# Performance work log

Hardware: AMD Instinct MI355X
Metric: run time of the kernel (lower is better)

Reference implementation:

```python
import jax, jax.numpy as jnp
import numpy as np

B, N, D, K = 4, 4096, 128, 20

def setup_inputs() -> dict:
    key = jax.random.key(0)
    k1, k2, k3 = jax.random.split(key, 3)
    s = 1.0 / np.sqrt(D)
    return {
        "x": jax.random.normal(k1, (B, N, D), dtype=jnp.float32),
        "Wq": jax.random.normal(k2, (D, D), dtype=jnp.float32) * s,
        "bq": jnp.zeros((D,), dtype=jnp.float32),
        "Wk": jax.random.normal(k3, (D, D), dtype=jnp.float32) * s,
        "bk": jnp.zeros((D,), dtype=jnp.float32),
    }

def reference(x, Wq, bq, Wk, bk):
    # Q/K projections: [B,N,D]
    Q = jnp.einsum('bnd,de->bne', x, Wq) + bq
    Kp = jnp.einsum('bnd,de->bne', x, Wk) + bk
    # scores: [B,N,N], scaled by sqrt(D)
    attn = jnp.einsum('bnd,bmd->bnm', Q, Kp) / jnp.sqrt(jnp.float32(D))
    # top-k along last dim -> binary mask via scatter
    _, topk_idx = jax.lax.top_k(attn, K)  # [B,N,K]
    bi = jnp.arange(B)[:, None, None]
    ni = jnp.arange(N)[None, :, None]
    mask = jnp.zeros_like(attn).at[bi, ni, topk_idx].set(1.0)
    # zero out non-topk entries, then full softmax over all N (zeros included,
    # matching the torch module exactly)
    sparse_attn = attn * mask
    out = jax.nn.softmax(sparse_attn, axis=-1)
    return out[..., None]  # [B,N,N,1]
```

## Files before the change

### kernel.cpp

```cpp
#include <hip/hip_runtime.h>

#define BN 4096
#define BD 128
#define NB 4
#define TOPK 20
#define CAND 96
#define EPS_U 0.9f

typedef float f32x16 __attribute__((ext_vector_type(16)));
typedef short bf16x8 __attribute__((ext_vector_type(8)));

__device__ inline unsigned short f2bf(float f) {
  unsigned int u = __float_as_uint(f);
  unsigned int r = (u + 0x7FFFu + ((u >> 16) & 1u)) >> 16;
  return (unsigned short)r;
}

__global__ __launch_bounds__(256) void proj_kernel(
    const float* __restrict__ x,
    const float* __restrict__ Wq, const float* __restrict__ bq,
    const float* __restrict__ Wk, const float* __restrict__ bk,
    double* __restrict__ Qd, double* __restrict__ Kd, unsigned short* __restrict__ Khi) {
  __shared__ double xs[32][129];
  const int tid = threadIdx.x;
  const long row0 = (long)blockIdx.x * 32;
  const float* xsrc = x + row0 * BD;
  for (int i = tid; i < 32 * BD; i += 256) xs[i >> 7][i & 127] = (double)xsrc[i];
  __syncthreads();

  const int e = tid & 127;
  const bool isK = tid >= 128;
  const float* W = isK ? Wk : Wq;
  const float* bias = isK ? bk : bq;
  double* Od = isK ? Kd : Qd;

  double acc[32];
  const double binit = (double)bias[e];
#pragma unroll
  for (int r = 0; r < 32; ++r) acc[r] = binit;

  for (int d = 0; d < BD; ++d) {
    const double wv = (double)W[d * BD + e];
#pragma unroll
    for (int r = 0; r < 32; ++r) acc[r] = fma(xs[r][d], wv, acc[r]);
  }

#pragma unroll
  for (int r = 0; r < 32; ++r) {
    const double a = acc[r];
    const long o = (row0 + r) * BD + e;
    Od[o] = a;
    if (isK) Khi[o] = f2bf((float)a);
  }
}

__global__ __launch_bounds__(512) void screen_kernel(
    const double* __restrict__ Qd, const unsigned short* __restrict__ Khi,
    unsigned short* __restrict__ Sbf) {
  __shared__ char sbuf[8][2560];

  const int tid = threadIdx.x;
  const int lane = tid & 63;
  const int w = tid >> 6;
  const int kt = w & 3, qt = w >> 2;
  const int c31 = lane & 31, hi = lane >> 5;

  const int blk = blockIdx.x;
  const int xcd = blk & 7;
  const int j = blk >> 3;
  const int combo = xcd * 2 + (j & 1);
  const int b = combo >> 2;
  const int kq = combo & 3;
  const int rg = j >> 1;
  const int rowbase = rg << 6;
  const int kvbase = kq << 10;

  const int qrow = qt * 32 + c31;
  const long grow = (long)b * BN + rowbase + qrow;

  bf16x8 bqf[8];
  {
    const double* qp = Qd + grow * BD + hi * 8;
#pragma unroll
    for (int ks = 0; ks < 8; ++ks) {
      bf16x8 pk;
#pragma unroll
      for (int jj = 0; jj < 8; ++jj) pk[jj] = (short)f2bf((float)qp[ks * 16 + jj]);
      bqf[ks] = pk;
    }
  }

  const unsigned short* kb = Khi + ((long)b * BN + kvbase + kt * 32 + c31) * BD + hi * 8;
  char* my = sbuf[w];
  const int wr = c31 * 80;

  const long gq = (long)b * BN + rowbase + qt * 32 + (lane >> 1);
  unsigned short* dstbase = Sbf + gq * BN + kvbase + kt * 32 + (lane & 1) * 16;
  const char* rdp = my + (lane >> 1) * 80 + (lane & 1) * 32;

  for (int step = 0; step < 8; ++step) {
    const unsigned short* kr = kb + (long)step * 128 * BD;
    f32x16 acc = {0.f, 0.f, 0.f, 0.f, 0.f, 0.f, 0.f, 0.f,
                  0.f, 0.f, 0.f, 0.f, 0.f, 0.f, 0.f, 0.f};
#pragma unroll
    for (int ks = 0; ks < 8; ++ks) {
      const bf16x8 a = *(const bf16x8*)(kr + ks * 16);
      acc = __builtin_amdgcn_mfma_f32_32x32x16_bf16(a, bqf[ks], acc, 0, 0, 0);
    }

#pragma unroll
    for (int p = 0; p < 4; ++p) {
      const unsigned int lo =
          (unsigned int)f2bf(acc[p * 4 + 0]) | ((unsigned int)f2bf(acc[p * 4 + 1]) << 16);
      const unsigned int hi2 =
          (unsigned int)f2bf(acc[p * 4 + 2]) | ((unsigned int)f2bf(acc[p * 4 + 3]) << 16);
      *(uint2*)(my + wr + p * 16 + hi * 8) = make_uint2(lo, hi2);
    }
    const uint4 r0 = *(const uint4*)(rdp);
    const uint4 r1 = *(const uint4*)(rdp + 16);
    unsigned short* dst = dstbase + step * 128;
    *(uint4*)dst = r0;
    *(uint4*)(dst + 8) = r1;
  }
}

__device__ inline float rescore_f64(const double2* __restrict__ kp2, const double2* __restrict__ q2) {
  double a0 = 0.0, a1 = 0.0, a2 = 0.0, a3 = 0.0;
#pragma unroll
  for (int i = 0; i < 64; i += 4) {
    a0 = fma(q2[i + 0].y, kp2[i + 0].y, fma(q2[i + 0].x, kp2[i + 0].x, a0));
    a1 = fma(q2[i + 1].y, kp2[i + 1].y, fma(q2[i + 1].x, kp2[i + 1].x, a1));
    a2 = fma(q2[i + 2].y, kp2[i + 2].y, fma(q2[i + 2].x, kp2[i + 2].x, a2));
    a3 = fma(q2[i + 3].y, kp2[i + 3].y, fma(q2[i + 3].x, kp2[i + 3].x, a3));
  }
  return (float)(((a0 + a1) + (a2 + a3)) * 8.8388347648318447e-02);
}

__device__ inline unsigned int fmono(float v) {
  const unsigned int u = __float_as_uint(v);
  return (u & 0x80000000u) ? ~u : (u | 0x80000000u);
}
__device__ inline float fdemono(unsigned int k) {
  const unsigned int u = (k & 0x80000000u) ? (k & 0x7fffffffu) : ~k;
  return __uint_as_float(u);
}

__global__ __launch_bounds__(256) void topk_kernel(
    const double* __restrict__ Qd, const double* __restrict__ Kd,
    const unsigned short* __restrict__ Sbf, unsigned int* __restrict__ rec) {
  __shared__ unsigned short listL[4][CAND];
  __shared__ unsigned int cntL[4];

  const int tid = threadIdx.x;
  const int lane = tid & 63;
  const int w = tid >> 6;
  const int blk = blockIdx.x;
  const int b = (blk & 7) >> 1;
  const int idx = ((blk >> 3) << 1) | (blk & 1);
  const long row = (long)b * BN + idx * 4 + w;

  const unsigned short* srow = Sbf + row * BN;

  uint4 v[8];
  float pm[8];
#pragma unroll
  for (int i = 0; i < 8; ++i) {
    v[i] = *(const uint4*)(srow + i * 512 + lane * 8);
    float m0 = -3.4e38f;
#pragma unroll
    for (int k = 0; k < 4; ++k) {
      const unsigned int u = (&v[i].x)[k];
      m0 = fmaxf(m0, fmaxf(__uint_as_float(u << 16), __uint_as_float(u & 0xFFFF0000u)));
    }
    pm[i] = m0;
  }
  float mymax = fmaxf(fmaxf(fmaxf(pm[0], pm[1]), fmaxf(pm[2], pm[3])),
                      fmaxf(fmaxf(pm[4], pm[5]), fmaxf(pm[6], pm[7])));

  float vb = mymax;
#pragma unroll
  for (int k = 2; k <= 64; k <<= 1) {
#pragma unroll
    for (int jj = k >> 1; jj > 0; jj >>= 1) {
      const float o = __shfl_xor(vb, jj);
      const bool keepmin = (((lane & k) == 0) == ((lane & jj) == 0));
      vb = keepmin ? fminf(vb, o) : fmaxf(vb, o);
    }
  }
  const float th = __shfl(vb, 44) - EPS_U;

  if (lane == 0) cntL[w] = 0;

#pragma unroll
  for (int i = 0; i < 8; ++i) {
#pragma unroll
    for (int k = 0; k < 4; ++k) {
      const unsigned int u = (&v[i].x)[k];
      const float f0 = __uint_as_float(u << 16);
      const float f1 = __uint_as_float(u & 0xFFFF0000u);
      const int col0 = i * 512 + lane * 8 + k * 2;
      if (f0 >= th) {
        const unsigned int p = atomicAdd(&cntL[w], 1u);
        if (p < CAND) listL[w][p] = (unsigned short)col0;
      }
      if (f1 >= th) {
        const unsigned int p = atomicAdd(&cntL[w], 1u);
        if (p < CAND) listL[w][p] = (unsigned short)(col0 + 1);
      }
    }
  }

  const int c = (int)min(cntL[w], (unsigned int)CAND);

  const double2* q2 = (const double2*)(Qd + row * BD);
  const double* kbd = Kd + (long)b * BN * BD;

  unsigned long long key0 = 0ull, key1 = 0ull;
  if (lane < c) {
    const int kv = (int)listL[w][lane];
    const float vv = rescore_f64((const double2*)(kbd + (long)kv * BD), q2);
    key0 = ((unsigned long long)fmono(vv) << 12) | (unsigned int)(4095 - kv);
  }
  if (lane + 64 < c) {
    const int kv = (int)listL[w][lane + 64];
    const float vv = rescore_f64((const double2*)(kbd + (long)kv * BD), q2);
    key1 = ((unsigned long long)fmono(vv) << 12) | (unsigned int)(4095 - kv);
  }

  unsigned int* rr = rec + row * 48;

  if (c <= 64) {
    unsigned long long kk = key0;
#pragma unroll
    for (int k = 2; k <= 64; k <<= 1) {
#pragma unroll
      for (int jj = k >> 1; jj > 0; jj >>= 1) {
        const unsigned long long o = __shfl_xor(kk, jj);
        const bool keepmin = (((lane & k) == 0) == ((lane & jj) == 0));
        kk = keepmin ? (o < kk ? o : kk) : (o > kk ? o : kk);
      }
    }
    const unsigned long long ktop = __shfl(kk, 63);
    const float m = fmaxf(fdemono((unsigned int)(ktop >> 12)), 0.0f);
    const float val = fdemono((unsigned int)(kk >> 12));
    const int col = 4095 - (int)(kk & 0xFFFull);
    const float e = (lane >= 44) ? expf(val - m) : 0.0f;
    float se = e;
#pragma unroll
    for (int off = 32; off; off >>= 1) se += __shfl_xor(se, off);
    const float Z = se + (float)(BN - TOPK) * expf(-m);
    if (lane >= 44) {
      const int r = 63 - lane;
      rr[r] = __float_as_uint(e / Z);
      rr[20 + r] = (unsigned int)col;
    }
    if (lane == 0) rr[40] = __float_as_uint(expf(-m) / Z);
  } else {
    if (key1 > key0) { const unsigned long long t = key0; key0 = key1; key1 = t; }
    float m = 0.0f, se = 0.0f;
    float myval = 0.0f;
    int mycol = 0;
    for (int it = 0; it < TOPK; ++it) {
      unsigned long long rk = key0;
      for (int off = 32; off; off >>= 1) {
        const unsigned long long ok = __shfl_xor(rk, off);
        rk = (ok > rk) ? ok : rk;
      }
      const float rv = fdemono((unsigned int)(rk >> 12));
      if (it == 0) m = fmaxf(rv, 0.0f);
      se += expf(rv - m);
      if (lane == it) { myval = rv; mycol = 4095 - (int)(rk & 0xFFFull); }
      if (key0 == rk) { key0 = key1; key1 = 0ull; }
    }
    const float Z = se + (float)(BN - TOPK) * expf(-m);
    if (lane < TOPK) {
      rr[lane] = __float_as_uint(expf(myval - m) / Z);
      rr[20 + lane] = (unsigned int)mycol;
    }
    if (lane == 0) rr[40] = __float_as_uint(expf(-m) / Z);
  }
}

__global__ __launch_bounds__(256) void fill_kernel(
    const unsigned int* __restrict__ rec, float* __restrict__ out) {
  __shared__ unsigned int bm[128];
  __shared__ float pv[TOPK];
  __shared__ int pc[TOPK];
  __shared__ float sc0;

  const int tid = threadIdx.x;
  const long row = blockIdx.x;
  const unsigned int* rr = rec + row * 48;

  if (tid < 128) bm[tid] = 0;
  __syncthreads();
  if (tid < TOPK) {
    pv[tid] = __uint_as_float(rr[tid]);
    const int col = (int)rr[20 + tid];
    pc[tid] = col;
    atomicOr(&bm[col >> 5], 1u << (col & 31));
  }
  if (tid == TOPK) sc0 = __uint_as_float(rr[40]);
  __syncthreads();

  const float c0 = sc0;
  const float4 cv = make_float4(c0, c0, c0, c0);
  float4* op = (float4*)(out + row * BN);

#pragma unroll
  for (int k = 0; k < 4; ++k) {
    const int j = tid + k * 256;
    const unsigned int bits = (bm[j >> 3] >> ((j & 7) * 4)) & 0xFu;
    if (bits == 0u) {
      op[j] = cv;
    } else {
      float4 v = cv;
      const int col0 = j * 4;
#pragma unroll
      for (int cmp = 0; cmp < 4; ++cmp) {
        if ((bits >> cmp) & 1u) {
          const int col = col0 + cmp;
          float pvv = c0;
          for (int i = 0; i < TOPK; ++i)
            if (pc[i] == col) pvv = pv[i];
          (&v.x)[cmp] = pvv;
        }
      }
      op[j] = v;
    }
  }
}

extern "C" void kernel_launch(void* const* d_in, const int* in_sizes, int n_in,
                              void* d_out, int out_size, void* d_ws, size_t ws_size,
                              hipStream_t stream) {
  const float* x  = (const float*)d_in[0];
  const float* Wq = (const float*)d_in[1];
  const float* bq = (const float*)d_in[2];
  const float* Wk = (const float*)d_in[3];
  const float* bk = (const float*)d_in[4];
  float* out = (float*)d_out;

  const long NE = (long)NB * BN * BD;
  const long NR = (long)NB * BN;
  double* Qd = (double*)d_ws;
  double* Kd = Qd + NE;
  unsigned short* Khi = (unsigned short*)(Kd + NE);
  unsigned short* Sbf = Khi + NE;
  unsigned int* rec = (unsigned int*)(Sbf + NR * BN);

  proj_kernel<<<NB * BN / 32, 256, 0, stream>>>(x, Wq, bq, Wk, bk, Qd, Kd, Khi);
  screen_kernel<<<1024, 512, 0, stream>>>(Qd, Khi, Sbf);
  topk_kernel<<<NR / 4, 256, 0, stream>>>(Qd, Kd, Sbf, rec);
  fill_kernel<<<NR, 256, 0, stream>>>(rec, out);
}
```

Before: 326.0 us.

## Fuse screening GEMM and top-k selection into one kernel with in-register threshold

Merges the bf16 MFMA screening kernel and the top-k rescoring kernel into a single kernel where each block owns 32 query rows across all 4096 keys. While computing scores, each lane keeps a running top-2, and these are pooled in shared memory and bitonic-sorted to derive the candidate threshold, replacing the separate full-row max pass. Candidate compaction now uses wave ballots and popcount instead of LDS atomics. The block still writes and then rereads the bf16 score rows. The grid shrinks to 512 blocks, so parallelism per block and launch occupancy change.

```diff
diff --git a/kernel.cpp b/kernel.cpp
--- a/kernel.cpp
+++ b/kernel.cpp
@@ -54,33 +54,49 @@
   }
 }
 
-__global__ __launch_bounds__(512) void screen_kernel(
-    const double* __restrict__ Qd, const unsigned short* __restrict__ Khi,
-    unsigned short* __restrict__ Sbf) {
+__device__ inline float rescore_f64(const double2* __restrict__ kp2, const double2* __restrict__ q2) {
+  double a0 = 0.0, a1 = 0.0, a2 = 0.0, a3 = 0.0;
+#pragma unroll
+  for (int i = 0; i < 64; i += 4) {
+    a0 = fma(q2[i + 0].y, kp2[i + 0].y, fma(q2[i + 0].x, kp2[i + 0].x, a0));
+    a1 = fma(q2[i + 1].y, kp2[i + 1].y, fma(q2[i + 1].x, kp2[i + 1].x, a1));
+    a2 = fma(q2[i + 2].y, kp2[i + 2].y, fma(q2[i + 2].x, kp2[i + 2].x, a2));
+    a3 = fma(q2[i + 3].y, kp2[i + 3].y, fma(q2[i + 3].x, kp2[i + 3].x, a3));
+  }
+  return (float)(((a0 + a1) + (a2 + a3)) * 8.8388347648318447e-02);
+}
+
+__device__ inline unsigned int fmono(float v) {
+  const unsigned int u = __float_as_uint(v);
+  return (u & 0x80000000u) ? ~u : (u | 0x80000000u);
+}
+__device__ inline float fdemono(unsigned int k) {
+  const unsigned int u = (k & 0x80000000u) ? (k & 0x7fffffffu) : ~k;
+  return __uint_as_float(u);
+}
+
+__global__ __launch_bounds__(512) void fused_kernel(
+    const double* __restrict__ Qd, const double* __restrict__ Kd,
+    const unsigned short* __restrict__ Khi,
+    unsigned short* __restrict__ Sbf, unsigned int* __restrict__ rec) {
   __shared__ char sbuf[8][2560];
+  __shared__ float pool[32][32];
+  __shared__ float tauL[32];
+  __shared__ unsigned short listL[8][CAND];
 
   const int tid = threadIdx.x;
   const int lane = tid & 63;
   const int w = tid >> 6;
-  const int kt = w & 3, qt = w >> 2;
   const int c31 = lane & 31, hi = lane >> 5;
 
   const int blk = blockIdx.x;
-  const int xcd = blk & 7;
-  const int j = blk >> 3;
-  const int combo = xcd * 2 + (j & 1);
-  const int b = combo >> 2;
-  const int kq = combo & 3;
-  const int rg = j >> 1;
-  const int rowbase = rg << 6;
-  const int kvbase = kq << 10;
-
-  const int qrow = qt * 32 + c31;
-  const long grow = (long)b * BN + rowbase + qrow;
+  const int b = (blk & 7) >> 1;
+  const int rg = ((blk >> 3) << 1) | (blk & 1);
+  const int rowbase = rg << 5;
 
   bf16x8 bqf[8];
   {
-    const double* qp = Qd + grow * BD + hi * 8;
+    const double* qp = Qd + ((long)b * BN + rowbase + c31) * BD + hi * 8;
 #pragma unroll
     for (int ks = 0; ks < 8; ++ks) {
       bf16x8 pk;
@@ -90,16 +106,18 @@
     }
   }
 
-  const unsigned short* kb = Khi + ((long)b * BN + kvbase + kt * 32 + c31) * BD + hi * 8;
+  const unsigned short* kb = Khi + ((long)b * BN + w * 512 + c31) * BD + hi * 8;
+
   char* my = sbuf[w];
   const int wr = c31 * 80;
-
-  const long gq = (long)b * BN + rowbase + qt * 32 + (lane >> 1);
-  unsigned short* dstbase = Sbf + gq * BN + kvbase + kt * 32 + (lane & 1) * 16;
+  unsigned short* dstbase = Sbf + ((long)b * BN + rowbase + (lane >> 1)) * BN
+                            + w * 512 + (lane & 1) * 16;
   const char* rdp = my + (lane >> 1) * 80 + (lane & 1) * 32;
 
-  for (int step = 0; step < 8; ++step) {
-    const unsigned short* kr = kb + (long)step * 128 * BD;
+  float t1 = -3.4e38f, t2 = -3.4e38f;
+
+  for (int t = 0; t < 16; ++t) {
+    const unsigned short* kr = kb + (long)t * 32 * BD;
     f32x16 acc = {0.f, 0.f, 0.f, 0.f, 0.f, 0.f, 0.f, 0.f,
                   0.f, 0.f, 0.f, 0.f, 0.f, 0.f, 0.f, 0.f};
 #pragma unroll
@@ -107,7 +125,13 @@
       const bf16x8 a = *(const bf16x8*)(kr + ks * 16);
       acc = __builtin_amdgcn_mfma_f32_32x32x16_bf16(a, bqf[ks], acc, 0, 0, 0);
     }
-
+#pragma unroll
+    for (int reg = 0; reg < 16; ++reg) {
+      const float s = acc[reg];
+      const float w1 = fmaxf(t1, s);
+      t2 = fmaxf(t2, fminf(t1, s));
+      t1 = w1;
+    }
 #pragma unroll
     for (int p = 0; p < 4; ++p) {
       const unsigned int lo =
@@ -118,166 +142,135 @@
     }
     const uint4 r0 = *(const uint4*)(rdp);
     const uint4 r1 = *(const uint4*)(rdp + 16);
-    unsigned short* dst = dstbase + step * 128;
+    unsigned short* dst = dstbase + t * 32;
     *(uint4*)dst = r0;
     *(uint4*)(dst + 8) = r1;
   }
-}
-
-__device__ inline float rescore_f64(const double2* __restrict__ kp2, const double2* __restrict__ q2) {
-  double a0 = 0.0, a1 = 0.0, a2 = 0.0, a3 = 0.0;
-#pragma unroll
-  for (int i = 0; i < 64; i += 4) {
-    a0 = fma(q2[i + 0].y, kp2[i + 0].y, fma(q2[i + 0].x, kp2[i + 0].x, a0));
-    a1 = fma(q2[i + 1].y, kp2[i + 1].y, fma(q2[i + 1].x, kp2[i + 1].x, a1));
-    a2 = fma(q2[i + 2].y, kp2[i + 2].y, fma(q2[i + 2].x, kp2[i + 2].x, a2));
-    a3 = fma(q2[i + 3].y, kp2[i + 3].y, fma(q2[i + 3].x, kp2[i + 3].x, a3));
-  }
-  return (float)(((a0 + a1) + (a2 + a3)) * 8.8388347648318447e-02);
-}
-
-__device__ inline unsigned int fmono(float v) {
-  const unsigned int u = __float_as_uint(v);
-  return (u & 0x80000000u) ? ~u : (u | 0x80000000u);
-}
-__device__ inline float fdemono(unsigned int k) {
-  const unsigned int u = (k & 0x80000000u) ? (k & 0x7fffffffu) : ~k;
-  return __uint_as_float(u);
-}
-
-__global__ __launch_bounds__(256) void topk_kernel(
-    const double* __restrict__ Qd, const double* __restrict__ Kd,
-    const unsigned short* __restrict__ Sbf, unsigned int* __restrict__ rec) {
-  __shared__ unsigned short listL[4][CAND];
-  __shared__ unsigned int cntL[4];
-
-  const int tid = threadIdx.x;
-  const int lane = tid & 63;
-  const int w = tid >> 6;
-  const int blk = blockIdx.x;
-  const int b = (blk & 7) >> 1;
-  const int idx = ((blk >> 3) << 1) | (blk & 1);
-  const long row = (long)b * BN + idx * 4 + w;
-
-  const unsigned short* srow = Sbf + row * BN;
-
-  uint4 v[8];
-  float pm[8];
-#pragma unroll
-  for (int i = 0; i < 8; ++i) {
-    v[i] = *(const uint4*)(srow + i * 512 + lane * 8);
-    float m0 = -3.4e38f;
-#pragma unroll
-    for (int k = 0; k < 4; ++k) {
-      const unsigned int u = (&v[i].x)[k];
-      m0 = fmaxf(m0, fmaxf(__uint_as_float(u << 16), __uint_as_float(u & 0xFFFF0000u)));
-    }
-    pm[i] = m0;
-  }
-  float mymax = fmaxf(fmaxf(fmaxf(pm[0], pm[1]), fmaxf(pm[2], pm[3])),
-                      fmaxf(fmaxf(pm[4], pm[5]), fmaxf(pm[6], pm[7])));
-
-  float vb = mymax;
-#pragma unroll
-  for (int k = 2; k <= 64; k <<= 1) {
-#pragma unroll
-    for (int jj = k >> 1; jj > 0; jj >>= 1) {
-      const float o = __shfl_xor(vb, jj);
-      const bool keepmin = (((lane & k) == 0) == ((lane & jj) == 0));
-      vb = keepmin ? fminf(vb, o) : fmaxf(vb, o);
-    }
-  }
-  const float th = __shfl(vb, 44) - EPS_U;
-
-  if (lane == 0) cntL[w] = 0;
-
-#pragma unroll
-  for (int i = 0; i < 8; ++i) {
-#pragma unroll
-    for (int k = 0; k < 4; ++k) {
-      const unsigned int u = (&v[i].x)[k];
-      const float f0 = __uint_as_float(u << 16);
-      const float f1 = __uint_as_float(u & 0xFFFF0000u);
-      const int col0 = i * 512 + lane * 8 + k * 2;
-      if (f0 >= th) {
-        const unsigned int p = atomicAdd(&cntL[w], 1u);
-        if (p < CAND) listL[w][p] = (unsigned short)col0;
-      }
-      if (f1 >= th) {
-        const unsigned int p = atomicAdd(&cntL[w], 1u);
-        if (p < CAND) listL[w][p] = (unsigned short)(col0 + 1);
-      }
-    }
-  }
-
-  const int c = (int)min(cntL[w], (unsigned int)CAND);
-
-  const double2* q2 = (const double2*)(Qd + row * BD);
+
+  pool[c31][(w * 2 + hi) * 2 + 0] = __uint_as_float(__float_as_uint(t1) & 0xFFFF0000u);
+  pool[c31][(w * 2 + hi) * 2 + 1] = __uint_as_float(__float_as_uint(t2) & 0xFFFF0000u);
+  __syncthreads();
+
+#pragma unroll
+  for (int p = 0; p < 2; ++p) {
+    const int row = w * 4 + p * 2 + hi;
+    float v = pool[row][c31];
+#pragma unroll
+    for (int k = 2; k <= 32; k <<= 1) {
+#pragma unroll
+      for (int jj = k >> 1; jj > 0; jj >>= 1) {
+        const float o = __shfl_xor(v, jj);
+        const bool keepmin = (((c31 & k) == 0) == ((c31 & jj) == 0));
+        v = keepmin ? fminf(v, o) : fmaxf(v, o);
+      }
+    }
+    if (c31 == 12) tauL[row] = v - EPS_U;
+  }
+  __syncthreads();
+
+  const unsigned long long lmask = (lane == 63) ? ~0ull >> 1 : (1ull << lane) - 1ull;
   const double* kbd = Kd + (long)b * BN * BD;
 
-  unsigned long long key0 = 0ull, key1 = 0ull;
-  if (lane < c) {
-    const int kv = (int)listL[w][lane];
-    const float vv = rescore_f64((const double2*)(kbd + (long)kv * BD), q2);
-    key0 = ((unsigned long long)fmono(vv) << 12) | (unsigned int)(4095 - kv);
-  }
-  if (lane + 64 < c) {
-    const int kv = (int)listL[w][lane + 64];
-    const float vv = rescore_f64((const double2*)(kbd + (long)kv * BD), q2);
-    key1 = ((unsigned long long)fmono(vv) << 12) | (unsigned int)(4095 - kv);
-  }
-
-  unsigned int* rr = rec + row * 48;
-
-  if (c <= 64) {
-    unsigned long long kk = key0;
-#pragma unroll
-    for (int k = 2; k <= 64; k <<= 1) {
-#pragma unroll
-      for (int jj = k >> 1; jj > 0; jj >>= 1) {
-        const unsigned long long o = __shfl_xor(kk, jj);
-        const bool keepmin = (((lane & k) == 0) == ((lane & jj) == 0));
-        kk = keepmin ? (o < kk ? o : kk) : (o > kk ? o : kk);
-      }
-    }
-    const unsigned long long ktop = __shfl(kk, 63);
-    const float m = fmaxf(fdemono((unsigned int)(ktop >> 12)), 0.0f);
-    const float val = fdemono((unsigned int)(kk >> 12));
-    const int col = 4095 - (int)(kk & 0xFFFull);
-    const float e = (lane >= 44) ? expf(val - m) : 0.0f;
-    float se = e;
-#pragma unroll
-    for (int off = 32; off; off >>= 1) se += __shfl_xor(se, off);
-    const float Z = se + (float)(BN - TOPK) * expf(-m);
-    if (lane >= 44) {
-      const int r = 63 - lane;
-      rr[r] = __float_as_uint(e / Z);
-      rr[20 + r] = (unsigned int)col;
-    }
-    if (lane == 0) rr[40] = __float_as_uint(expf(-m) / Z);
-  } else {
-    if (key1 > key0) { const unsigned long long t = key0; key0 = key1; key1 = t; }
-    float m = 0.0f, se = 0.0f;
-    float myval = 0.0f;
-    int mycol = 0;
-    for (int it = 0; it < TOPK; ++it) {
-      unsigned long long rk = key0;
-      for (int off = 32; off; off >>= 1) {
-        const unsigned long long ok = __shfl_xor(rk, off);
-        rk = (ok > rk) ? ok : rk;
-      }
-      const float rv = fdemono((unsigned int)(rk >> 12));
-      if (it == 0) m = fmaxf(rv, 0.0f);
-      se += expf(rv - m);
-      if (lane == it) { myval = rv; mycol = 4095 - (int)(rk & 0xFFFull); }
-      if (key0 == rk) { key0 = key1; key1 = 0ull; }
-    }
-    const float Z = se + (float)(BN - TOPK) * expf(-m);
-    if (lane < TOPK) {
-      rr[lane] = __float_as_uint(expf(myval - m) / Z);
-      rr[20 + lane] = (unsigned int)mycol;
-    }
-    if (lane == 0) rr[40] = __float_as_uint(expf(-m) / Z);
+  for (int rr2 = 0; rr2 < 4; ++rr2) {
+    const int row = w * 4 + rr2;
+    const long grow = (long)b * BN + rowbase + row;
+    const unsigned short* srow = Sbf + grow * BN;
+    const float th = tauL[row];
+
+    uint4 v[8];
+#pragma unroll
+    for (int i = 0; i < 8; ++i) v[i] = *(const uint4*)(srow + i * 512 + lane * 8);
+
+    unsigned int base = 0;
+#pragma unroll
+    for (int i = 0; i < 8; ++i) {
+#pragma unroll
+      for (int k = 0; k < 4; ++k) {
+        const unsigned int u = (&v[i].x)[k];
+        const float f0 = __uint_as_float(u << 16);
+        const float f1 = __uint_as_float(u & 0xFFFF0000u);
+        const int col0 = i * 512 + lane * 8 + k * 2;
+        const unsigned long long b0 = __ballot(f0 >= th);
+        if (f0 >= th) {
+          const unsigned int p = base + (unsigned int)__popcll(b0 & lmask);
+          if (p < CAND) listL[w][p] = (unsigned short)col0;
+        }
+        base += (unsigned int)__popcll(b0);
+        const unsigned long long b1 = __ballot(f1 >= th);
+        if (f1 >= th) {
+          const unsigned int p = base + (unsigned int)__popcll(b1 & lmask);
+          if (p < CAND) listL[w][p] = (unsigned short)(col0 + 1);
+        }
+        base += (unsigned int)__popcll(b1);
+      }
+    }
+    const int c = (int)min(base, (unsigned int)CAND);
+
+    const double2* q2 = (const double2*)(Qd + grow * BD);
+    unsigned long long key0 = 0ull, key1 = 0ull;
+    if (lane < c) {
+      const int kv = (int)listL[w][lane];
+      const float vv = rescore_f64((const double2*)(kbd + (long)kv * BD), q2);
+      key0 = ((unsigned long long)fmono(vv) << 12) | (unsigned int)(4095 - kv);
+    }
+    if (lane + 64 < c) {
+      const int kv = (int)listL[w][lane + 64];
+      const float vv = rescore_f64((const double2*)(kbd + (long)kv * BD), q2);
+      key1 = ((unsigned long long)fmono(vv) << 12) | (unsigned int)(4095 - kv);
+    }
+
+    unsigned int* rr = rec + grow * 48;
+
+    if (c <= 64) {
+      unsigned long long kk = key0;
+#pragma unroll
+      for (int k = 2; k <= 64; k <<= 1) {
+#pragma unroll
+        for (int jj = k >> 1; jj > 0; jj >>= 1) {
+          const unsigned long long o = __shfl_xor(kk, jj);
+          const bool keepmin = (((lane & k) == 0) == ((lane & jj) == 0));
+          kk = keepmin ? (o < kk ? o : kk) : (o > kk ? o : kk);
+        }
+      }
+      const unsigned long long ktop = __shfl(kk, 63);
+      const float m = fmaxf(fdemono((unsigned int)(ktop >> 12)), 0.0f);
+      const float val = fdemono((unsigned int)(kk >> 12));
+      const int col = 4095 - (int)(kk & 0xFFFull);
+      const float e = (lane >= 44) ? expf(val - m) : 0.0f;
+      float se = e;
+#pragma unroll
+      for (int off = 32; off; off >>= 1) se += __shfl_xor(se, off);
+      const float Z = se + (float)(BN - TOPK) * expf(-m);
+      if (lane >= 44) {
+        const int r = 63 - lane;
+        rr[r] = __float_as_uint(e / Z);
+        rr[20 + r] = (unsigned int)col;
+      }
+      if (lane == 0) rr[40] = __float_as_uint(expf(-m) / Z);
+    } else {
+      if (key1 > key0) { const unsigned long long t = key0; key0 = key1; key1 = t; }
+      float m = 0.0f, se = 0.0f;
+      float myval = 0.0f;
+      int mycol = 0;
+      for (int it = 0; it < TOPK; ++it) {
+        unsigned long long rk = key0;
+        for (int off = 32; off; off >>= 1) {
+          const unsigned long long ok = __shfl_xor(rk, off);
+          rk = (ok > rk) ? ok : rk;
+        }
+        const float rv = fdemono((unsigned int)(rk >> 12));
+        if (it == 0) m = fmaxf(rv, 0.0f);
+        se += expf(rv - m);
+        if (lane == it) { myval = rv; mycol = 4095 - (int)(rk & 0xFFFull); }
+        if (key0 == rk) { key0 = key1; key1 = 0ull; }
+      }
+      const float Z = se + (float)(BN - TOPK) * expf(-m);
+      if (lane < TOPK) {
+        rr[lane] = __float_as_uint(expf(myval - m) / Z);
+        rr[20 + lane] = (unsigned int)mycol;
+      }
+      if (lane == 0) rr[40] = __float_as_uint(expf(-m) / Z);
+    }
   }
 }
 
@@ -350,7 +343,6 @@
   unsigned int* rec = (unsigned int*)(Sbf + NR * BN);
 
   proj_kernel<<<NB * BN / 32, 256, 0, stream>>>(x, Wq, bq, Wk, bk, Qd, Kd, Khi);
-  screen_kernel<<<1024, 512, 0, stream>>>(Qd, Khi, Sbf);
-  topk_kernel<<<NR / 4, 256, 0, stream>>>(Qd, Kd, Sbf, rec);
+  fused_kernel<<<512, 512, 0, stream>>>(Qd, Kd, Khi, Sbf, rec);
   fill_kernel<<<NR, 256, 0, stream>>>(rec, out);
 }
```

New measurement: 322.8 us. Within noise of the previous version (-1.0%).
